# Kernel optimization log

Hardware: AMD Instinct MI355X
Metric: run time of the kernel (lower is better)

The kernel has to match this reference:

```python
import jax, jax.numpy as jnp
import numpy as np

B, L, D, H = 16, 1024, 768, 12
PHD = D // H  # per-head dim = 64


def setup_inputs() -> dict:
    key = jax.random.key(0)
    ks = jax.random.split(key, 6)
    s = 0.02  # small init scale (xavier-like magnitude)
    return {
        "embeddings": jax.random.normal(ks[0], (B, L, D), jnp.float32),
        "pre_w": jax.random.normal(ks[1], (D, D), jnp.float32) * s,
        "pre_b": jnp.zeros((D,), jnp.float32),
        "psfs": jax.random.normal(ks[2], (H, 2 * L - 1, PHD), jnp.float32) * s,
        "post_w": jax.random.normal(ks[3], (D, D), jnp.float32) * s,
        "post_b": jnp.zeros((D,), jnp.float32),
        "sparse_mat": jax.random.normal(ks[4], (L, L), jnp.float32) * s,
        "ln_g": jnp.ones((D,), jnp.float32),
        "ln_b": jnp.zeros((D,), jnp.float32),
    }


def _spectral_norm(W, n_iters=1, eps=1e-12):
    # torch spectral_norm: power iteration with detached u, v; sigma = u^T W v
    u = jnp.ones((W.shape[0],), W.dtype) / jnp.sqrt(jnp.asarray(W.shape[0], W.dtype))
    for _ in range(n_iters):
        v = W.T @ u
        v = v / (jnp.linalg.norm(v) + eps)
        u = W @ v
        u = u / (jnp.linalg.norm(u) + eps)
    u = jax.lax.stop_gradient(u)
    v = jax.lax.stop_gradient(v)
    sigma = u @ (W @ v)
    return W / sigma


def reference(embeddings, pre_w, pre_b, psfs, post_w, post_b, sparse_mat, ln_g, ln_b):
    # pre-projection
    x = embeddings @ pre_w.T + pre_b                       # (B, L, D)
    # zero-pad along seq to 2L-1 and split heads
    xp = jnp.pad(x, ((0, 0), (0, L - 1), (0, 0)))          # (B, 2L-1, D)
    xp = xp.reshape(B, 2 * L - 1, H, PHD).transpose(0, 2, 1, 3)  # (B, H, 2L-1, d)
    # causal PSF mask: keep first L taps, zero the rest (zeros still enter softmax, as in torch)
    causal = (jnp.arange(2 * L - 1) < L)[None, :, None]
    psf = jnp.where(causal, psfs, 0.0)                     # (H, 2L-1, d)
    psf = jax.nn.softmax(psf, axis=1)
    # 2D circular convolution via FFT over (seq, head_dim)
    conv = jnp.fft.ifftn(jnp.fft.fftn(psf, axes=(1, 2))[None] * jnp.fft.fftn(xp, axes=(2, 3)), axes=(2, 3))
    conv = jnp.real(conv)[:, :, :L, :]                     # (B, H, L, d)
    conv = jax.nn.gelu(conv, approximate=False).transpose(0, 2, 1, 3).reshape(B, L, D)
    conv_emb = conv @ post_w.T + post_b
    # sparse branch: spectrally-normalized, causal-masked dense mixing matrix
    sp = jnp.tril(_spectral_norm(sparse_mat))              # (L, L)
    sparse_emb = jnp.einsum('st,btd->bsd', sp, x)
    # dropout is identity (eval), keep_prob = 1.0; residual + LayerNorm(eps=1e-12)
    y = conv_emb + sparse_emb + embeddings
    mu = jnp.mean(y, axis=-1, keepdims=True)
    var = jnp.mean((y - mu) ** 2, axis=-1, keepdims=True)
    return (y - mu) * jax.lax.rsqrt(var + 1e-12) * ln_g + ln_b
```

## Files before the change

kernel.cpp:

```cpp
#include <hip/hip_runtime.h>
#include <math.h>

#define Bn 16
#define Ln 1024
#define Dn 768
#define Hn 12
#define PHDn 64
#define NK 33
#define NHK (Hn * NK)
#define TWOPI_64 0.09817477042468103f

typedef short s16x8 __attribute__((ext_vector_type(8)));
typedef float f32x4 __attribute__((ext_vector_type(4)));
typedef unsigned short u16x4 __attribute__((ext_vector_type(4)));

__device__ __forceinline__ unsigned short f2bf(float f) {
    unsigned int u = __float_as_uint(f);
    unsigned int r = (u + 0x7FFFu + ((u >> 16) & 1u)) >> 16;
    return (unsigned short)r;
}
__device__ __forceinline__ float bf2f(unsigned short s) {
    unsigned int u = ((unsigned int)s) << 16;
    return __uint_as_float(u);
}
__device__ __forceinline__ float2 cmul(float2 a, float2 b) {
    return make_float2(a.x * b.x - a.y * b.y, a.x * b.y + a.y * b.x);
}
__device__ __forceinline__ unsigned int packbf(float re, float im) {
    return (unsigned int)f2bf(re) | ((unsigned int)f2bf(im) << 16);
}
__device__ __forceinline__ float2 unpackbf(unsigned int v) {
    return make_float2(bf2f((unsigned short)(v & 0xffff)), bf2f((unsigned short)(v >> 16)));
}

#define SW(j) ((j) ^ (((j) >> 2) & 12) ^ (((j) >> 6) & 3))

static const size_t O_P    = 0;
static const size_t O_PSFH = 786432;
static const size_t O_PART = 1376256;
static const size_t O_QH   = 1597440;
static const size_t O_X    = 1598240;
static const size_t O_XH   = 14181152;
static const size_t O_YH   = 27157280;
static const size_t O_SPE  = 40146080;
static const size_t O_V    = 52728992;
static const size_t O_UR   = 52730016;
static const size_t O_SIG  = 52731040;

__global__ __launch_bounds__(256) void k_psf_softmax(const float* __restrict__ psfs,
                                                     float* __restrict__ p,
                                                     float* __restrict__ q) {
    int he = blockIdx.x;
    int h = he >> 6, e = he & 63;
    int tid = threadIdx.x;
    float ev[4];
    float s = 0.f;
#pragma unroll
    for (int i = 0; i < 4; ++i) {
        int t = tid + 256 * i;
        float v = psfs[((size_t)h * 2047 + t) * 64 + e];
        ev[i] = expf(v);
        s += ev[i];
    }
    __shared__ float red[256];
    red[tid] = s; __syncthreads();
    for (int st = 128; st > 0; st >>= 1) {
        if (tid < st) red[tid] += red[tid + st];
        __syncthreads();
    }
    float denom = red[0] + 1023.0f;
    float inv = 1.0f / denom;
#pragma unroll
    for (int i = 0; i < 4; ++i) {
        int t = tid + 256 * i;
        p[((size_t)h * 1024 + t) * 64 + e] = ev[i] * inv;
    }
    if (tid == 0) q[he] = inv;
}

__global__ __launch_bounds__(256) void k_psf_dft(const float* __restrict__ p,
                                                 float* __restrict__ psfh) {
    int blk = blockIdx.x;
    int h = blk >> 8, tb = blk & 255;
    int t0 = tb * 4;
    int tid = threadIdx.x;
    int w = tid >> 6, lane = tid & 63;
    __shared__ float pv[4][64], cc[64], ssn[64];
    if (tid < 64) {
        float ang = TWOPI_64 * tid;
        cc[tid] = cosf(ang); ssn[tid] = sinf(ang);
    }
    pv[w][lane] = p[((size_t)h * 1024 + t0 + w) * 64 + lane];
    __syncthreads();
    if (lane < NK) {
        float re = 0.f, im = 0.f;
#pragma unroll 8
        for (int e = 0; e < 64; ++e) {
            int j = (lane * e) & 63;
            float v = pv[w][e];
            re += v * cc[j];
            im -= v * ssn[j];
        }
        size_t o = (((size_t)h * NK + lane) * 1024 + t0 + w) * 2;
        psfh[o] = re; psfh[o + 1] = im;
    }
}

__global__ __launch_bounds__(64) void k_q_dft(const float* __restrict__ q,
                                              float* __restrict__ qh) {
    int h = blockIdx.x;
    int tid = threadIdx.x;
    __shared__ float qv[64], cc[64], ssn[64];
    qv[tid] = q[h * 64 + tid];
    float ang = TWOPI_64 * tid;
    cc[tid] = cosf(ang); ssn[tid] = sinf(ang);
    __syncthreads();
    if (tid < NK) {
        float re = 0.f, im = 0.f;
        for (int e = 0; e < 64; ++e) {
            int j = (tid * e) & 63;
            re += qv[e] * cc[j];
            im -= qv[e] * ssn[j];
        }
        qh[(h * NK + tid) * 2] = re;
        qh[(h * NK + tid) * 2 + 1] = im;
    }
}

__device__ __forceinline__ void build_twiddles(float2* tw, int tid) {
#pragma unroll
    for (int it = 0; it < 2; ++it) {
        int j = tid + it * 256;
        float a = (float)j * 3.0679615757712823e-3f;
        float sv, cv;
        __sincosf(a, &sv, &cv);
        tw[j] = make_float2(cv, -sv);
    }
}

__device__ __forceinline__ void fft_pair(const float2* __restrict__ X,
                                         float2* __restrict__ Y,
                                         const float2* __restrict__ tw,
                                         int tid, int m) {
#pragma unroll
    for (int it = 0; it < 2; ++it) {
        int i = tid + it * 256;
        int r = i & (m - 1);
        int am = i - r;
        float2 w1 = tw[am];
        float2 w1b = make_float2(w1.y, -w1.x);
        float2 w2 = cmul(w1, w1);
        float2 x0 = X[SW(i)], x1 = X[SW(i + 512)], x2 = X[SW(i + 1024)], x3 = X[SW(i + 1536)];
        float2 y0 = make_float2(x0.x + x2.x, x0.y + x2.y);
        float2 y1 = cmul(make_float2(x0.x - x2.x, x0.y - x2.y), w1);
        float2 y2 = make_float2(x1.x + x3.x, x1.y + x3.y);
        float2 y3 = cmul(make_float2(x1.x - x3.x, x1.y - x3.y), w1b);
        int o = 4 * am + r;
        Y[SW(o)] = make_float2(y0.x + y2.x, y0.y + y2.y);
        Y[SW(o + m)] = make_float2(y1.x + y3.x, y1.y + y3.y);
        Y[SW(o + 2 * m)] = cmul(make_float2(y0.x - y2.x, y0.y - y2.y), w2);
        Y[SW(o + 3 * m)] = cmul(make_float2(y1.x - y3.x, y1.y - y3.y), w2);
    }
}

__global__ __launch_bounds__(256) void k_tap_fft(const float* __restrict__ psfh,
                                                 const float* __restrict__ qh,
                                                 float* __restrict__ phf) {
    __shared__ float2 A[2048], B[2048], tw[512];
    int hk = blockIdx.x, tid = threadIdx.x;
    build_twiddles(tw, tid);
    float2 qv = make_float2(qh[hk * 2], qh[hk * 2 + 1]);
    const float2* Pg = (const float2*)(psfh + (size_t)hk * 2048);
    __syncthreads();
#pragma unroll
    for (int it = 0; it < 2; ++it) {
        int i = tid + it * 256;
        float2 x0 = Pg[i], x1 = Pg[i + 512];
        float2 x2 = (i == 0) ? make_float2(0.f, 0.f) : qv;
        float2 x3 = qv;
        float2 w1 = tw[i];
        float2 w1b = make_float2(w1.y, -w1.x);
        float2 w2 = cmul(w1, w1);
        float2 y0 = make_float2(x0.x + x2.x, x0.y + x2.y);
        float2 y1 = cmul(make_float2(x0.x - x2.x, x0.y - x2.y), w1);
        float2 y2 = make_float2(x1.x + x3.x, x1.y + x3.y);
        float2 y3 = cmul(make_float2(x1.x - x3.x, x1.y - x3.y), w1b);
        int o = 4 * i;
        A[SW(o)] = make_float2(y0.x + y2.x, y0.y + y2.y);
        A[SW(o + 1)] = make_float2(y1.x + y3.x, y1.y + y3.y);
        A[SW(o + 2)] = cmul(make_float2(y0.x - y2.x, y0.y - y2.y), w2);
        A[SW(o + 3)] = cmul(make_float2(y1.x - y3.x, y1.y - y3.y), w2);
    }
    __syncthreads();
    fft_pair(A, B, tw, tid, 4);   __syncthreads();
    fft_pair(B, A, tw, tid, 16);  __syncthreads();
    fft_pair(A, B, tw, tid, 64);  __syncthreads();
    fft_pair(B, A, tw, tid, 256); __syncthreads();
    float2* out = (float2*)(phf + (size_t)hk * 4096);
#pragma unroll
    for (int it = 0; it < 4; ++it) {
        int t = tid + it * 256;
        float2 lo = A[SW(t)], hi = A[SW(t + 1024)];
        out[t] = make_float2(lo.x + hi.x, lo.y + hi.y);
        out[t + 1024] = make_float2(lo.x - hi.x, lo.y - hi.y);
    }
}

__global__ __launch_bounds__(256) void k_conv_fft(const unsigned int* __restrict__ XHb,
                                                  const float* __restrict__ PHF,
                                                  unsigned int* __restrict__ YHb) {
    __shared__ float2 A[2048], B[2048], tw[512];
    int bhk = blockIdx.x, tid = threadIdx.x;
    int hk = bhk % NHK;
    build_twiddles(tw, tid);
    const unsigned int* Xg = XHb + (size_t)bhk * 1024;
    __syncthreads();
#pragma unroll
    for (int it = 0; it < 2; ++it) {
        int i = tid + it * 256;
        float2 x0 = unpackbf(Xg[i]);
        float2 x1 = unpackbf(Xg[i + 512]);
        float2 w1 = tw[i];
        float2 w1b = make_float2(w1.y, -w1.x);
        float2 w2 = cmul(w1, w1);
        float2 y1 = cmul(x0, w1);
        float2 y3 = cmul(x1, w1b);
        int o = 4 * i;
        A[SW(o)] = make_float2(x0.x + x1.x, x0.y + x1.y);
        A[SW(o + 1)] = make_float2(y1.x + y3.x, y1.y + y3.y);
        A[SW(o + 2)] = cmul(make_float2(x0.x - x1.x, x0.y - x1.y), w2);
        A[SW(o + 3)] = cmul(make_float2(y1.x - y3.x, y1.y - y3.y), w2);
    }
    __syncthreads();
    fft_pair(A, B, tw, tid, 4);   __syncthreads();
    fft_pair(B, A, tw, tid, 16);  __syncthreads();
    fft_pair(A, B, tw, tid, 64);  __syncthreads();
    fft_pair(B, A, tw, tid, 256); __syncthreads();
    const float2* P = (const float2*)(PHF + (size_t)hk * 4096);
    float2 q[8];
#pragma unroll
    for (int it = 0; it < 4; ++it) {
        int t = tid + it * 256;
        float2 lo = A[SW(t)], hi = A[SW(t + 1024)];
        float2 fl = make_float2(lo.x + hi.x, lo.y + hi.y);
        float2 fh = make_float2(lo.x - hi.x, lo.y - hi.y);
        float2 vl = cmul(fl, P[t]);
        float2 vh = cmul(fh, P[t + 1024]);
        q[it] = make_float2(vl.x, -vl.y);
        q[it + 4] = make_float2(vh.x, -vh.y);
    }
#pragma unroll
    for (int it = 0; it < 2; ++it) {
        int i = tid + it * 256;
        float2 x0 = q[it], x1 = q[it + 2], x2 = q[it + 4], x3 = q[it + 6];
        float2 w1 = tw[i];
        float2 w1b = make_float2(w1.y, -w1.x);
        float2 w2 = cmul(w1, w1);
        float2 y0 = make_float2(x0.x + x2.x, x0.y + x2.y);
        float2 y1 = cmul(make_float2(x0.x - x2.x, x0.y - x2.y), w1);
        float2 y2 = make_float2(x1.x + x3.x, x1.y + x3.y);
        float2 y3 = cmul(make_float2(x1.x - x3.x, x1.y - x3.y), w1b);
        int o = 4 * i;
        B[SW(o)] = make_float2(y0.x + y2.x, y0.y + y2.y);
        B[SW(o + 1)] = make_float2(y1.x + y3.x, y1.y + y3.y);
        B[SW(o + 2)] = cmul(make_float2(y0.x - y2.x, y0.y - y2.y), w2);
        B[SW(o + 3)] = cmul(make_float2(y1.x - y3.x, y1.y - y3.y), w2);
    }
    __syncthreads();
    fft_pair(B, A, tw, tid, 4);   __syncthreads();
    fft_pair(A, B, tw, tid, 16);  __syncthreads();
    fft_pair(B, A, tw, tid, 64);  __syncthreads();
    fft_pair(A, B, tw, tid, 256); __syncthreads();
    unsigned int* Yg = YHb + (size_t)bhk * 1024;
    const float inv_n = 1.0f / 2048.0f;
#pragma unroll
    for (int it = 0; it < 4; ++it) {
        int s = tid + it * 256;
        float2 lo = B[SW(s)], hi = B[SW(s + 1024)];
        Yg[s] = packbf((lo.x + hi.x) * inv_n, -(lo.y + hi.y) * inv_n);
    }
}

__global__ __launch_bounds__(64) void k_build_wf1(unsigned short* __restrict__ W) {
    int m = blockIdx.x;
    int d = threadIdx.x;
    float val = 0.f;
    if (m < 66) {
        int k = m >> 1, od = m & 1;
        int j = (k * d) & 63;
        float ang = TWOPI_64 * (float)j;
        val = od ? -sinf(ang) : cosf(ang);
    }
    W[m * 64 + d] = f2bf(val);
}

__global__ __launch_bounds__(64) void k_build_wi1(unsigned short* __restrict__ W) {
    int m = blockIdx.x;
    int c = threadIdx.x;
    float val = 0.f;
    if (m < 64) {
        int d = m;
        int k, od;
        float ck;
        if (c == 0)      { k = 0;  od = 0; ck = 1.f / 64.f; }
        else if (c == 1) { k = 32; od = 0; ck = 1.f / 64.f; }
        else             { k = c >> 1; od = c & 1; ck = 2.f / 64.f; }
        int j = (k * d) & 63;
        float ang = TWOPI_64 * (float)j;
        val = od ? -sinf(ang) * ck : cosf(ang) * ck;
    }
    W[m * 64 + c] = f2bf(val);
}

__device__ __forceinline__ void mfma_core64(const unsigned short* __restrict__ gA0,
                                            const unsigned short* __restrict__ gB0,
                                            int nkt,
                                            unsigned short* __restrict__ As,
                                            unsigned short* __restrict__ Bs,
                                            int tid, int lane, int wr, int wc,
                                            f32x4 acc[4][4]) {
    int r0 = tid >> 1, hs = (tid & 1) << 2;
    int wbase = r0 * 64;
    int swr = r0 & 7;
    int kg = lane >> 4, cl = lane & 15;
    int fra[8], frb[8];
#pragma unroll
    for (int kk = 0; kk < 2; ++kk)
#pragma unroll
        for (int i = 0; i < 4; ++i) {
            int ra = wr * 64 + i * 16 + cl;
            fra[kk * 4 + i] = ra * 64 + (((kk * 4 + kg) ^ (ra & 7)) << 3);
            int rb = wc * 64 + i * 16 + cl;
            frb[kk * 4 + i] = rb * 64 + (((kk * 4 + kg) ^ (rb & 7)) << 3);
        }
    s16x8 a[4], b[4];
#pragma unroll
    for (int l = 0; l < 4; ++l) {
        a[l] = *(const s16x8*)(gA0 + l * 8);
        b[l] = *(const s16x8*)(gB0 + l * 8);
    }
    for (int kt = 0; kt < nkt; ++kt) {
        __syncthreads();
#pragma unroll
        for (int l = 0; l < 4; ++l) {
            *(s16x8*)&As[wbase + (((hs + l) ^ swr) << 3)] = a[l];
            *(s16x8*)&Bs[wbase + (((hs + l) ^ swr) << 3)] = b[l];
        }
        __syncthreads();
        if (kt + 1 < nkt) {
            size_t ko = (size_t)(kt + 1) * 64;
#pragma unroll
            for (int l = 0; l < 4; ++l) {
                a[l] = *(const s16x8*)(gA0 + ko + l * 8);
                b[l] = *(const s16x8*)(gB0 + ko + l * 8);
            }
        }
#pragma unroll
        for (int kk = 0; kk < 2; ++kk) {
            s16x8 af[4], bfr[4];
#pragma unroll
            for (int i = 0; i < 4; ++i) af[i] = *(const s16x8*)&As[fra[kk * 4 + i]];
#pragma unroll
            for (int i = 0; i < 4; ++i) bfr[i] = *(const s16x8*)&Bs[frb[kk * 4 + i]];
#pragma unroll
            for (int mi = 0; mi < 4; ++mi)
#pragma unroll
                for (int ni = 0; ni < 4; ++ni)
                    acc[mi][ni] = __builtin_amdgcn_mfma_f32_16x16x32_bf16(af[mi], bfr[ni], acc[mi][ni], 0, 0, 0);
        }
    }
}

__global__ __launch_bounds__(512) void k_mfma_proj(const unsigned short* __restrict__ A,
                                                   const unsigned short* __restrict__ W,
                                                   const float* __restrict__ bias,
                                                   unsigned short* __restrict__ C) {
    const int K = Dn, N = Dn;
    int n0 = blockIdx.x * 256, m0 = blockIdx.y * 128;
    int tid = threadIdx.x;
    int lane = tid & 63, wave = tid >> 6;
    int wr = wave >> 2, wc = wave & 3;
    __shared__ __align__(16) unsigned short As[8192], Bs[16384];
    f32x4 acc[4][4] = {};
    int ra0 = tid >> 2, sa0 = (tid & 3) * 2;
    int rb0 = tid >> 1, sb0 = (tid & 1) * 4;
    const unsigned short* gA = A + (size_t)(m0 + ra0) * K + sa0 * 8;
    const unsigned short* gB = W + (size_t)(n0 + rb0) * K + sb0 * 8;
    int kg = lane >> 4, cl = lane & 15;
    int fra[8], frb[8];
#pragma unroll
    for (int kk = 0; kk < 2; ++kk)
#pragma unroll
        for (int i = 0; i < 4; ++i) {
            int ra = wr * 64 + i * 16 + cl;
            fra[kk * 4 + i] = ra * 64 + (((kk * 4 + kg) ^ (ra & 7)) << 3);
            int rb = wc * 64 + i * 16 + cl;
            frb[kk * 4 + i] = rb * 64 + (((kk * 4 + kg) ^ (rb & 7)) << 3);
        }
    s16x8 a[2], b[4];
#pragma unroll
    for (int l = 0; l < 2; ++l) a[l] = *(const s16x8*)(gA + l * 8);
#pragma unroll
    for (int l = 0; l < 4; ++l) b[l] = *(const s16x8*)(gB + l * 8);
    const int nkt = K >> 6;
    for (int kt = 0; kt < nkt; ++kt) {
        __syncthreads();
#pragma unroll
        for (int l = 0; l < 2; ++l)
            *(s16x8*)&As[ra0 * 64 + (((sa0 + l) ^ (ra0 & 7)) << 3)] = a[l];
#pragma unroll
        for (int l = 0; l < 4; ++l)
            *(s16x8*)&Bs[rb0 * 64 + (((sb0 + l) ^ (rb0 & 7)) << 3)] = b[l];
        __syncthreads();
        if (kt + 1 < nkt) {
            size_t ko = (size_t)(kt + 1) * 64;
#pragma unroll
            for (int l = 0; l < 2; ++l) a[l] = *(const s16x8*)(gA + ko + l * 8);
#pragma unroll
            for (int l = 0; l < 4; ++l) b[l] = *(const s16x8*)(gB + ko + l * 8);
        }
#pragma unroll
        for (int kk = 0; kk < 2; ++kk) {
            s16x8 af[4], bfr[4];
#pragma unroll
            for (int i = 0; i < 4; ++i) af[i] = *(const s16x8*)&As[fra[kk * 4 + i]];
#pragma unroll
            for (int i = 0; i < 4; ++i) bfr[i] = *(const s16x8*)&Bs[frb[kk * 4 + i]];
#pragma unroll
            for (int mi = 0; mi < 4; ++mi)
#pragma unroll
                for (int ni = 0; ni < 4; ++ni)
                    acc[mi][ni] = __builtin_amdgcn_mfma_f32_16x16x32_bf16(af[mi], bfr[ni], acc[mi][ni], 0, 0, 0);
        }
    }
#pragma unroll
    for (int ni = 0; ni < 4; ++ni) {
        int gn = n0 + wc * 64 + ni * 16 + cl;
        float bv = bias[gn];
#pragma unroll
        for (int mi = 0; mi < 4; ++mi) {
            int gm = m0 + wr * 64 + mi * 16 + kg * 4;
            f32x4 v = acc[mi][ni];
#pragma unroll
            for (int ri = 0; ri < 4; ++ri)
                C[(size_t)(gm + ri) * N + gn] = f2bf(v[ri] + bv);
        }
    }
}

__global__ __launch_bounds__(256) void k_mfma_dft_h(const unsigned short* __restrict__ Wf1,
                                                    const unsigned short* __restrict__ Xb,
                                                    unsigned int* __restrict__ XHb) {
    int n0 = blockIdx.x * 128;
    int h = blockIdx.y;
    int tid = threadIdx.x;
    int lane = tid & 63, wave = tid >> 6;
    int wr = wave >> 1, wc = wave & 1;
    __shared__ __align__(16) unsigned short As[8192], Bs[8192];
    f32x4 acc[4][4] = {};
    int r0 = tid >> 1, hs = (tid & 1) << 2;
    const unsigned short* gA0 = Wf1 + r0 * 64 + hs * 8;
    const unsigned short* gB0 = Xb + (size_t)(n0 + r0) * Dn + h * 64 + hs * 8;
    mfma_core64(gA0, gB0, 1, As, Bs, tid, lane, wr, wc, acc);
    int kg = lane >> 4, cl = lane & 15;
#pragma unroll
    for (int ni = 0; ni < 4; ++ni) {
        int gn = n0 + wc * 64 + ni * 16 + cl;
        int b = gn >> 10, u = gn & 1023;
#pragma unroll
        for (int mi = 0; mi < 4; ++mi) {
            int gmb = wr * 64 + mi * 16 + kg * 4;
            f32x4 v = acc[mi][ni];
#pragma unroll
            for (int rp = 0; rp < 2; ++rp) {
                int m = gmb + rp * 2;
                if (m < 66) {
                    size_t plane = (size_t)(b * Hn + h) * NK + (m >> 1);
                    XHb[plane * 1024 + u] = packbf(v[rp * 2], v[rp * 2 + 1]);
                }
            }
        }
    }
}

__global__ __launch_bounds__(256) void k_transpose_yh(const unsigned int* __restrict__ YHb,
                                                      unsigned short* __restrict__ YT) {
    int ut = blockIdx.x & 7;
    int h = (blockIdx.x >> 3) % 12;
    int b = blockIdx.x / 96;
    int u0 = ut * 128;
    __shared__ unsigned short T[128 * 66];
    int tid = threadIdx.x;
    int planeBase = (b * Hn + h) * NK;
#pragma unroll
    for (int i = 0; i < 17; ++i) {
        int idx = tid + i * 256;
        if (idx < 4224) {
            int k = idx >> 7, uo = idx & 127;
            unsigned int v = YHb[(size_t)(planeBase + k) * 1024 + u0 + uo];
            T[uo * 66 + 2 * k] = (unsigned short)(v & 0xffff);
            T[uo * 66 + 2 * k + 1] = (unsigned short)(v >> 16);
        }
    }
    __syncthreads();
    unsigned int* out = (unsigned int*)YT;
#pragma unroll
    for (int i = 0; i < 16; ++i) {
        int idx = tid + i * 256;
        int uo = idx >> 5, w = idx & 31;
        unsigned int lo, hi;
        if (w == 0) {
            lo = T[uo * 66 + 0];
            hi = T[uo * 66 + 64];
        } else {
            lo = T[uo * 66 + 2 * w];
            hi = T[uo * 66 + 2 * w + 1];
        }
        size_t r = (size_t)b * 1024 + u0 + uo;
        out[r * 384 + h * 32 + w] = lo | (hi << 16);
    }
}

__global__ __launch_bounds__(256) void k_mfma_idft_h(const unsigned short* __restrict__ YT,
                                                     const unsigned short* __restrict__ Wi1,
                                                     unsigned short* __restrict__ G) {
    int m0 = blockIdx.x * 128;
    int h = blockIdx.y;
    int tid = threadIdx.x;
    int lane = tid & 63, wave = tid >> 6;
    int wr = wave >> 1, wc = wave & 1;
    __shared__ __align__(16) unsigned short As[8192], Bs[8192];
    f32x4 acc[4][4] = {};
    int r0 = tid >> 1, hs = (tid & 1) << 2;
    const unsigned short* gA0 = YT + (size_t)(m0 + r0) * Dn + h * 64 + hs * 8;
    const unsigned short* gB0 = Wi1 + r0 * 64 + hs * 8;
    mfma_core64(gA0, gB0, 1, As, Bs, tid, lane, wr, wc, acc);
    int kg = lane >> 4, cl = lane & 15;
#pragma unroll
    for (int ni = 0; ni < 4; ++ni) {
        int gn = wc * 64 + ni * 16 + cl;
        if (gn < 64) {
#pragma unroll
            for (int mi = 0; mi < 4; ++mi) {
                int gm = m0 + wr * 64 + mi * 16 + kg * 4;
                f32x4 v = acc[mi][ni];
#pragma unroll
                for (int ri = 0; ri < 4; ++ri) {
                    float c = v[ri];
                    float g = c * 0.5f * (1.0f + erff(c * 0.70710678118f));
                    G[(size_t)(gm + ri) * Dn + h * 64 + gn] = f2bf(g);
                }
            }
        }
    }
}

__global__ __launch_bounds__(256) void k_mfma_sparse(const unsigned short* __restrict__ SP,
                                                     const unsigned short* __restrict__ XT,
                                                     const float* __restrict__ sigbuf,
                                                     unsigned short* __restrict__ C) {
    int bx = blockIdx.x;
    int mt = bx & 7, nt = (bx >> 3) % 6, b = bx / 48;
    int m0 = mt * 128, n0 = nt * 128;
    const unsigned short* Xb = XT + (size_t)b * Dn * Ln;
    unsigned short* Cb = C + (size_t)b * Ln * Dn;
    int tid = threadIdx.x;
    int lane = tid & 63, wave = tid >> 6;
    int wr = wave >> 1, wc = wave & 1;
    __shared__ __align__(16) unsigned short As[8192], Bs[8192];
    f32x4 acc[4][4] = {};
    int r0 = tid >> 1, hs = (tid & 1) << 2;
    const unsigned short* gA0 = SP + (size_t)(m0 + r0) * Ln + hs * 8;
    const unsigned short* gB0 = Xb + (size_t)(n0 + r0) * Ln + hs * 8;
    mfma_core64(gA0, gB0, 2 * mt + 2, As, Bs, tid, lane, wr, wc, acc);
    float invs = sigbuf[0];
    int kg = lane >> 4, cl = lane & 15;
#pragma unroll
    for (int ni = 0; ni < 4; ++ni) {
        int gn = n0 + wc * 64 + ni * 16 + cl;
#pragma unroll
        for (int mi = 0; mi < 4; ++mi) {
            int gm = m0 + wr * 64 + mi * 16 + kg * 4;
            f32x4 v = acc[mi][ni];
#pragma unroll
            for (int ri = 0; ri < 4; ++ri)
                Cb[(size_t)(gm + ri) * Dn + gn] = f2bf(v[ri] * invs);
        }
    }
}

__global__ __launch_bounds__(256) void k_cvt_bf16(const float* __restrict__ in,
                                                  unsigned short* __restrict__ out, int n4) {
    int i = blockIdx.x * 256 + threadIdx.x;
    if (i < n4) {
        float4 v = ((const float4*)in)[i];
        u16x4 o;
        o[0] = f2bf(v.x); o[1] = f2bf(v.y); o[2] = f2bf(v.z); o[3] = f2bf(v.w);
        *(u16x4*)&out[(size_t)i * 4] = o;
    }
}

__global__ __launch_bounds__(256) void k_cvt_sp(const float* __restrict__ SP,
                                                unsigned short* __restrict__ O) {
    int s = blockIdx.x;
    int t0 = threadIdx.x * 4;
    float4 v = *(const float4*)&SP[(size_t)s * 1024 + t0];
    u16x4 o;
    o[0] = (t0 + 0 <= s) ? f2bf(v.x) : 0;
    o[1] = (t0 + 1 <= s) ? f2bf(v.y) : 0;
    o[2] = (t0 + 2 <= s) ? f2bf(v.z) : 0;
    o[3] = (t0 + 3 <= s) ? f2bf(v.w) : 0;
    *(u16x4*)&O[(size_t)s * 1024 + t0] = o;
}

__global__ __launch_bounds__(256) void k_transpose_x(const unsigned short* __restrict__ X,
                                                     unsigned short* __restrict__ XT) {
    int d0 = blockIdx.x * 64, t0 = blockIdx.y * 64, b = blockIdx.z;
    const unsigned short* Xb = X + (size_t)b * Ln * Dn;
    unsigned short* Tb = XT + (size_t)b * Dn * Ln;
    __shared__ unsigned short tile[64 * 65];
    int tx = threadIdx.x & 63, ty = threadIdx.x >> 6;
#pragma unroll
    for (int i = 0; i < 16; ++i) {
        int t = ty + i * 4;
        tile[t * 65 + tx] = Xb[(size_t)(t0 + t) * Dn + d0 + tx];
    }
    __syncthreads();
#pragma unroll
    for (int i = 0; i < 16; ++i) {
        int d = ty + i * 4;
        Tb[(size_t)(d0 + d) * Ln + t0 + tx] = tile[tx * 65 + d];
    }
}

__global__ __launch_bounds__(256) void k_sn_colsum(const float* __restrict__ Wm,
                                                   float* __restrict__ partial) {
    int b = blockIdx.x;
    int tid = threadIdx.x;
    int c0 = tid * 4;
    float4 s = make_float4(0.f, 0.f, 0.f, 0.f);
#pragma unroll
    for (int i = 0; i < 16; ++i) {
        float4 v = *(const float4*)&Wm[(size_t)(b * 16 + i) * 1024 + c0];
        s.x += v.x; s.y += v.y; s.z += v.z; s.w += v.w;
    }
    *(float4*)&partial[(size_t)b * 1024 + c0] = s;
}

__global__ __launch_bounds__(1024) void k_sn_v2(const float* __restrict__ partial,
                                                float* __restrict__ v) {
    int j = threadIdx.x;
    float s = 0.f;
#pragma unroll 8
    for (int i = 0; i < 64; ++i) s += partial[(size_t)i * 1024 + j];
    s *= 0.03125f;
    __shared__ float red[1024];
    red[j] = s * s; __syncthreads();
    for (int st = 512; st > 0; st >>= 1) {
        if (j < st) red[j] += red[j + st];
        __syncthreads();
    }
    float nrm = sqrtf(red[0]);
    v[j] = s / (nrm + 1e-12f);
}

__global__ __launch_bounds__(64) void k_sn_u(const float* __restrict__ Wm,
                                             const float* __restrict__ v,
                                             float* __restrict__ ur) {
    int i = blockIdx.x;
    int lane = threadIdx.x;
    float s = 0.f;
    for (int j = lane; j < 1024; j += 64) s += Wm[(size_t)i * 1024 + j] * v[j];
#pragma unroll
    for (int off = 32; off > 0; off >>= 1) s += __shfl_down(s, off);
    if (lane == 0) ur[i] = s;
}

__global__ __launch_bounds__(1024) void k_sn_sigma(const float* __restrict__ ur,
                                                   float* __restrict__ sig) {
    int i = threadIdx.x;
    __shared__ float red[1024];
    float u = ur[i];
    red[i] = u * u; __syncthreads();
    for (int st = 512; st > 0; st >>= 1) {
        if (i < st) red[i] += red[i + st];
        __syncthreads();
    }
    if (i == 0) {
        float ss = red[0];
        float sigma = ss / (sqrtf(ss) + 1e-12f);
        sig[0] = 1.0f / sigma;
    }
}

__global__ __launch_bounds__(256) void k_final_ln(const unsigned short* __restrict__ CE,
                                                  const unsigned short* __restrict__ SE,
                                                  const float* __restrict__ EMB,
                                                  const float* __restrict__ g,
                                                  const float* __restrict__ be,
                                                  float* __restrict__ out) {
    int r = blockIdx.x;
    int tid = threadIdx.x;
    float y[3];
    float s = 0.f;
#pragma unroll
    for (int i = 0; i < 3; ++i) {
        int o = tid + i * 256;
        size_t idx = (size_t)r * 768 + o;
        y[i] = bf2f(CE[idx]) + bf2f(SE[idx]) + EMB[idx];
        s += y[i];
    }
    __shared__ float red[256];
    red[tid] = s; __syncthreads();
    for (int st = 128; st > 0; st >>= 1) {
        if (tid < st) red[tid] += red[tid + st];
        __syncthreads();
    }
    float mu = red[0] * (1.f / 768.f);
    __syncthreads();
    float vs = 0.f;
#pragma unroll
    for (int i = 0; i < 3; ++i) { float d = y[i] - mu; vs += d * d; }
    red[tid] = vs; __syncthreads();
    for (int st = 128; st > 0; st >>= 1) {
        if (tid < st) red[tid] += red[tid + st];
        __syncthreads();
    }
    float var = red[0] * (1.f / 768.f);
    float rstd = rsqrtf(var + 1e-12f);
#pragma unroll
    for (int i = 0; i < 3; ++i) {
        int o = tid + i * 256;
        size_t idx = (size_t)r * 768 + o;
        out[idx] = (y[i] - mu) * rstd * g[o] + be[o];
    }
}

extern "C" void kernel_launch(void* const* d_in, const int* in_sizes, int n_in,
                              void* d_out, int out_size, void* d_ws, size_t ws_size,
                              hipStream_t stream) {
    const float* emb     = (const float*)d_in[0];
    const float* pre_w   = (const float*)d_in[1];
    const float* pre_b   = (const float*)d_in[2];
    const float* psfs    = (const float*)d_in[3];
    const float* post_w  = (const float*)d_in[4];
    const float* post_b  = (const float*)d_in[5];
    const float* spmat   = (const float*)d_in[6];
    const float* ln_g    = (const float*)d_in[7];
    const float* ln_b    = (const float*)d_in[8];
    float* out = (float*)d_out;
    float* ws = (float*)d_ws;

    float* p      = ws + O_P;
    float* psfh   = ws + O_PSFH;
    float* part   = ws + O_PART;
    float* qh     = ws + O_QH;
    float* q      = ws + O_SIG + 8;
    unsigned int* XHb = (unsigned int*)(ws + O_XH);
    unsigned int* YHb = (unsigned int*)(ws + O_YH);
    float* phf    = ws + O_SPE;
    float* v      = ws + O_V;
    float* urw    = ws + O_UR;
    float* sig    = ws + O_SIG;

    unsigned short* x_bf      = (unsigned short*)(ws + O_X);
    unsigned short* Wf1       = (unsigned short*)(ws + O_X + 6291456);
    unsigned short* Wi1       = (unsigned short*)(ws + O_X + 6295552);
    unsigned short* YT        = (unsigned short*)(ws + O_XH);
    unsigned short* xT_bf     = (unsigned short*)(ws + O_XH);
    unsigned short* emb_bf    = (unsigned short*)(ws + O_YH);
    unsigned short* CE_bf     = (unsigned short*)(ws + O_YH);
    unsigned short* spe_bf    = (unsigned short*)(ws + O_SPE);
    unsigned short* G_bf      = (unsigned short*)(ws + O_SPE + 3145728);
    unsigned short* SP_bf     = (unsigned short*)(ws + O_P);
    unsigned short* pre_w_bf  = (unsigned short*)(ws + O_PSFH);
    unsigned short* post_w_bf = (unsigned short*)(ws + O_PSFH + 294912);

    k_psf_softmax<<<Hn * 64, 256, 0, stream>>>(psfs, p, q);
    k_psf_dft<<<Hn * 256, 256, 0, stream>>>(p, psfh);
    k_q_dft<<<Hn, 64, 0, stream>>>(q, qh);
    k_tap_fft<<<NHK, 256, 0, stream>>>(psfh, qh, phf);

    k_sn_colsum<<<64, 256, 0, stream>>>(spmat, part);
    k_sn_v2<<<1, 1024, 0, stream>>>(part, v);
    k_sn_u<<<1024, 64, 0, stream>>>(spmat, v, urw);
    k_sn_sigma<<<1, 1024, 0, stream>>>(urw, sig);

    k_cvt_sp<<<1024, 256, 0, stream>>>(spmat, SP_bf);
    k_cvt_bf16<<<576, 256, 0, stream>>>(pre_w, pre_w_bf, 147456);
    k_cvt_bf16<<<576, 256, 0, stream>>>(post_w, post_w_bf, 147456);
    k_cvt_bf16<<<12288, 256, 0, stream>>>(emb, emb_bf, 3145728);
    k_build_wf1<<<128, 64, 0, stream>>>(Wf1);
    k_build_wi1<<<128, 64, 0, stream>>>(Wi1);

    k_mfma_proj<<<dim3(3, 128), 512, 0, stream>>>(emb_bf, pre_w_bf, pre_b, x_bf);

    k_mfma_dft_h<<<dim3(128, Hn), 256, 0, stream>>>(Wf1, x_bf, XHb);

    k_conv_fft<<<Bn * NHK, 256, 0, stream>>>(XHb, phf, YHb);

    k_transpose_yh<<<Bn * Hn * 8, 256, 0, stream>>>(YHb, YT);

    k_mfma_idft_h<<<dim3(128, Hn), 256, 0, stream>>>(YT, Wi1, G_bf);

    k_transpose_x<<<dim3(12, 16, Bn), 256, 0, stream>>>(x_bf, xT_bf);

    k_mfma_proj<<<dim3(3, 128), 512, 0, stream>>>(G_bf, post_w_bf, post_b, CE_bf);

    k_mfma_sparse<<<768, 256, 0, stream>>>(SP_bf, xT_bf, sig, spe_bf);

    k_final_ln<<<Bn * Ln, 256, 0, stream>>>(CE_bf, spe_bf, emb, ln_g, ln_b, out);
}
```

Measured before the change: 315.4 us.

## Restructure conv FFT into radix-8 register passes with padded single shared buffer

Rewrites the per-(b,h,k) 2048-point FFT convolution kernel to use radix-8 register-resident passes (three stages plus a final radix-4) instead of radix-4 ping-pong passes through two shared arrays. This cuts the number of shared-memory round trips and barriers per FFT. The A/B ping-pong becomes one shared buffer with skew padding in place of the XOR swizzle, which lowers LDS footprint and may allow more resident blocks. The inverse pass computes only the first 1024 outputs it needs. Register pressure per thread rises, which may hurt occupancy.

```diff
diff --git a/kernel.cpp b/kernel.cpp
--- a/kernel.cpp
+++ b/kernel.cpp
@@ -26,6 +26,8 @@
 __device__ __forceinline__ float2 cmul(float2 a, float2 b) {
     return make_float2(a.x * b.x - a.y * b.y, a.x * b.y + a.y * b.x);
 }
+__device__ __forceinline__ float2 cadd(float2 a, float2 b) { return make_float2(a.x + b.x, a.y + b.y); }
+__device__ __forceinline__ float2 csub(float2 a, float2 b) { return make_float2(a.x - b.x, a.y - b.y); }
 __device__ __forceinline__ unsigned int packbf(float re, float im) {
     return (unsigned int)f2bf(re) | ((unsigned int)f2bf(im) << 16);
 }
@@ -34,6 +36,7 @@
 }
 
 #define SW(j) ((j) ^ (((j) >> 2) & 12) ^ (((j) >> 6) & 3))
+#define PD(j) ((j) + ((j) >> 4))
 
 static const size_t O_P    = 0;
 static const size_t O_PSFH = 786432;
@@ -151,15 +154,15 @@
         float2 w1b = make_float2(w1.y, -w1.x);
         float2 w2 = cmul(w1, w1);
         float2 x0 = X[SW(i)], x1 = X[SW(i + 512)], x2 = X[SW(i + 1024)], x3 = X[SW(i + 1536)];
-        float2 y0 = make_float2(x0.x + x2.x, x0.y + x2.y);
-        float2 y1 = cmul(make_float2(x0.x - x2.x, x0.y - x2.y), w1);
-        float2 y2 = make_float2(x1.x + x3.x, x1.y + x3.y);
-        float2 y3 = cmul(make_float2(x1.x - x3.x, x1.y - x3.y), w1b);
+        float2 y0 = cadd(x0, x2);
+        float2 y1 = cmul(csub(x0, x2), w1);
+        float2 y2 = cadd(x1, x3);
+        float2 y3 = cmul(csub(x1, x3), w1b);
         int o = 4 * am + r;
-        Y[SW(o)] = make_float2(y0.x + y2.x, y0.y + y2.y);
-        Y[SW(o + m)] = make_float2(y1.x + y3.x, y1.y + y3.y);
-        Y[SW(o + 2 * m)] = cmul(make_float2(y0.x - y2.x, y0.y - y2.y), w2);
-        Y[SW(o + 3 * m)] = cmul(make_float2(y1.x - y3.x, y1.y - y3.y), w2);
+        Y[SW(o)] = cadd(y0, y2);
+        Y[SW(o + m)] = cadd(y1, y3);
+        Y[SW(o + 2 * m)] = cmul(csub(y0, y2), w2);
+        Y[SW(o + 3 * m)] = cmul(csub(y1, y3), w2);
     }
 }
 
@@ -181,15 +184,15 @@
         float2 w1 = tw[i];
         float2 w1b = make_float2(w1.y, -w1.x);
         float2 w2 = cmul(w1, w1);
-        float2 y0 = make_float2(x0.x + x2.x, x0.y + x2.y);
-        float2 y1 = cmul(make_float2(x0.x - x2.x, x0.y - x2.y), w1);
-        float2 y2 = make_float2(x1.x + x3.x, x1.y + x3.y);
-        float2 y3 = cmul(make_float2(x1.x - x3.x, x1.y - x3.y), w1b);
+        float2 y0 = cadd(x0, x2);
+        float2 y1 = cmul(csub(x0, x2), w1);
+        float2 y2 = cadd(x1, x3);
+        float2 y3 = cmul(csub(x1, x3), w1b);
         int o = 4 * i;
-        A[SW(o)] = make_float2(y0.x + y2.x, y0.y + y2.y);
-        A[SW(o + 1)] = make_float2(y1.x + y3.x, y1.y + y3.y);
-        A[SW(o + 2)] = cmul(make_float2(y0.x - y2.x, y0.y - y2.y), w2);
-        A[SW(o + 3)] = cmul(make_float2(y1.x - y3.x, y1.y - y3.y), w2);
+        A[SW(o)] = cadd(y0, y2);
+        A[SW(o + 1)] = cadd(y1, y3);
+        A[SW(o + 2)] = cmul(csub(y0, y2), w2);
+        A[SW(o + 3)] = cmul(csub(y1, y3), w2);
     }
     __syncthreads();
     fft_pair(A, B, tw, tid, 4);   __syncthreads();
@@ -201,83 +204,146 @@
     for (int it = 0; it < 4; ++it) {
         int t = tid + it * 256;
         float2 lo = A[SW(t)], hi = A[SW(t + 1024)];
-        out[t] = make_float2(lo.x + hi.x, lo.y + hi.y);
-        out[t + 1024] = make_float2(lo.x - hi.x, lo.y - hi.y);
-    }
+        out[t] = cadd(lo, hi);
+        out[t + 1024] = csub(lo, hi);
+    }
+}
+
+__device__ __forceinline__ void triple_tail(float2 z0, float2 z1, float2 z2, float2 z3,
+                                            float2 zz0, float2 zz1, float2 zz2, float2 zz3,
+                                            float2 w2, float2 w4, float2* o) {
+    float2 w2b = make_float2(w2.y, -w2.x);
+    float2 a0 = cadd(z0, z2),   a2 = cmul(csub(z0, z2), w2);
+    float2 b0 = cadd(z1, z3),   b2 = cmul(csub(z1, z3), w2b);
+    float2 a1 = cadd(zz0, zz2), a3 = cmul(csub(zz0, zz2), w2);
+    float2 b1 = cadd(zz1, zz3), b3 = cmul(csub(zz1, zz3), w2b);
+    o[0] = cadd(a0, b0); o[4] = cmul(csub(a0, b0), w4);
+    o[1] = cadd(a1, b1); o[5] = cmul(csub(a1, b1), w4);
+    o[2] = cadd(a2, b2); o[6] = cmul(csub(a2, b2), w4);
+    o[3] = cadd(a3, b3); o[7] = cmul(csub(a3, b3), w4);
+}
+
+__device__ __forceinline__ void fft_triple(const float2* x, float2 w10, float2 w11, float2* o) {
+    float2 w10b = make_float2(w10.y, -w10.x), w11b = make_float2(w11.y, -w11.x);
+    float2 w2 = cmul(w10, w10), w4 = cmul(w2, w2);
+    float2 z0 = cadd(x[0], x[4]), z1 = cadd(x[1], x[5]);
+    float2 z2 = cadd(x[2], x[6]), z3 = cadd(x[3], x[7]);
+    float2 zz0 = cmul(csub(x[0], x[4]), w10);
+    float2 zz1 = cmul(csub(x[1], x[5]), w11);
+    float2 zz2 = cmul(csub(x[2], x[6]), w10b);
+    float2 zz3 = cmul(csub(x[3], x[7]), w11b);
+    triple_tail(z0, z1, z2, z3, zz0, zz1, zz2, zz3, w2, w4, o);
 }
 
 __global__ __launch_bounds__(256) void k_conv_fft(const unsigned int* __restrict__ XHb,
                                                   const float* __restrict__ PHF,
                                                   unsigned int* __restrict__ YHb) {
-    __shared__ float2 A[2048], B[2048], tw[512];
+    __shared__ float2 S[2176], tw[512];
     int bhk = blockIdx.x, tid = threadIdx.x;
     int hk = bhk % NHK;
     build_twiddles(tw, tid);
     const unsigned int* Xg = XHb + (size_t)bhk * 1024;
-    __syncthreads();
+    float2 x[8], o[8];
+#pragma unroll
+    for (int k = 0; k < 4; ++k) x[k] = unpackbf(Xg[tid + 256 * k]);
+    __syncthreads();
+    {
+        float2 w10 = tw[tid], w11 = tw[tid + 256];
+        float2 w10b = make_float2(w10.y, -w10.x), w11b = make_float2(w11.y, -w11.x);
+        float2 w2 = cmul(w10, w10), w4 = cmul(w2, w2);
+        float2 zz0 = cmul(x[0], w10), zz1 = cmul(x[1], w11);
+        float2 zz2 = cmul(x[2], w10b), zz3 = cmul(x[3], w11b);
+        triple_tail(x[0], x[1], x[2], x[3], zz0, zz1, zz2, zz3, w2, w4, o);
+    }
+#pragma unroll
+    for (int k = 0; k < 8; ++k) S[PD(8 * tid + k)] = o[k];
+    __syncthreads();
+    {
+        int r = tid & 7, am = tid - r;
+#pragma unroll
+        for (int k = 0; k < 8; ++k) x[k] = S[PD(tid + 256 * k)];
+        __syncthreads();
+        fft_triple(x, tw[am], tw[am + 256], o);
+        int base = 8 * am + r;
+#pragma unroll
+        for (int k = 0; k < 8; ++k) S[PD(base + 8 * k)] = o[k];
+    }
+    __syncthreads();
+    {
+        int r = tid & 63, am = tid - r;
+#pragma unroll
+        for (int k = 0; k < 8; ++k) x[k] = S[PD(tid + 256 * k)];
+        __syncthreads();
+        fft_triple(x, tw[am], tw[am + 256], o);
+        int base = 8 * am + r;
+#pragma unroll
+        for (int k = 0; k < 8; ++k) S[PD(base + 64 * k)] = o[k];
+    }
+    __syncthreads();
+    const float2* P = (const float2*)(PHF + (size_t)hk * 4096);
+    float2 v[8];
 #pragma unroll
     for (int it = 0; it < 2; ++it) {
-        int i = tid + it * 256;
-        float2 x0 = unpackbf(Xg[i]);
-        float2 x1 = unpackbf(Xg[i + 512]);
-        float2 w1 = tw[i];
-        float2 w1b = make_float2(w1.y, -w1.x);
-        float2 w2 = cmul(w1, w1);
-        float2 y1 = cmul(x0, w1);
-        float2 y3 = cmul(x1, w1b);
-        int o = 4 * i;
-        A[SW(o)] = make_float2(x0.x + x1.x, x0.y + x1.y);
-        A[SW(o + 1)] = make_float2(y1.x + y3.x, y1.y + y3.y);
-        A[SW(o + 2)] = cmul(make_float2(x0.x - x1.x, x0.y - x1.y), w2);
-        A[SW(o + 3)] = cmul(make_float2(y1.x - y3.x, y1.y - y3.y), w2);
-    }
-    __syncthreads();
-    fft_pair(A, B, tw, tid, 4);   __syncthreads();
-    fft_pair(B, A, tw, tid, 16);  __syncthreads();
-    fft_pair(A, B, tw, tid, 64);  __syncthreads();
-    fft_pair(B, A, tw, tid, 256); __syncthreads();
-    const float2* P = (const float2*)(PHF + (size_t)hk * 4096);
-    float2 q[8];
-#pragma unroll
-    for (int it = 0; it < 4; ++it) {
-        int t = tid + it * 256;
-        float2 lo = A[SW(t)], hi = A[SW(t + 1024)];
-        float2 fl = make_float2(lo.x + hi.x, lo.y + hi.y);
-        float2 fh = make_float2(lo.x - hi.x, lo.y - hi.y);
-        float2 vl = cmul(fl, P[t]);
-        float2 vh = cmul(fh, P[t + 1024]);
-        q[it] = make_float2(vl.x, -vl.y);
-        q[it + 4] = make_float2(vh.x, -vh.y);
-    }
-#pragma unroll
-    for (int it = 0; it < 2; ++it) {
-        int i = tid + it * 256;
-        float2 x0 = q[it], x1 = q[it + 2], x2 = q[it + 4], x3 = q[it + 6];
-        float2 w1 = tw[i];
-        float2 w1b = make_float2(w1.y, -w1.x);
-        float2 w2 = cmul(w1, w1);
-        float2 y0 = make_float2(x0.x + x2.x, x0.y + x2.y);
-        float2 y1 = cmul(make_float2(x0.x - x2.x, x0.y - x2.y), w1);
-        float2 y2 = make_float2(x1.x + x3.x, x1.y + x3.y);
-        float2 y3 = cmul(make_float2(x1.x - x3.x, x1.y - x3.y), w1b);
-        int o = 4 * i;
-        B[SW(o)] = make_float2(y0.x + y2.x, y0.y + y2.y);
-        B[SW(o + 1)] = make_float2(y1.x + y3.x, y1.y + y3.y);
-        B[SW(o + 2)] = cmul(make_float2(y0.x - y2.x, y0.y - y2.y), w2);
-        B[SW(o + 3)] = cmul(make_float2(y1.x - y3.x, y1.y - y3.y), w2);
-    }
-    __syncthreads();
-    fft_pair(B, A, tw, tid, 4);   __syncthreads();
-    fft_pair(A, B, tw, tid, 16);  __syncthreads();
-    fft_pair(B, A, tw, tid, 64);  __syncthreads();
-    fft_pair(A, B, tw, tid, 256); __syncthreads();
+        int i2 = tid + 256 * it;
+        float2 g0 = S[PD(i2)], g1 = S[PD(i2 + 512)], g2 = S[PD(i2 + 1024)], g3 = S[PD(i2 + 1536)];
+        float2 y0 = cadd(g0, g2), y1 = csub(g0, g2);
+        float2 y2 = cadd(g1, g3);
+        float2 d13 = csub(g1, g3);
+        float2 y3 = make_float2(d13.y, -d13.x);
+        float2 F0 = cadd(y0, y2);
+        float2 F1 = cadd(y1, y3);
+        float2 F2 = csub(y0, y2);
+        float2 F3 = csub(y1, y3);
+        float2 V0 = cmul(F0, P[i2]);
+        float2 V1 = cmul(F1, P[i2 + 512]);
+        float2 V2 = cmul(F2, P[i2 + 1024]);
+        float2 V3 = cmul(F3, P[i2 + 1536]);
+        v[it]     = make_float2(V0.x, -V0.y);
+        v[it + 2] = make_float2(V1.x, -V1.y);
+        v[it + 4] = make_float2(V2.x, -V2.y);
+        v[it + 6] = make_float2(V3.x, -V3.y);
+    }
+    __syncthreads();
+    fft_triple(v, tw[tid], tw[tid + 256], o);
+#pragma unroll
+    for (int k = 0; k < 8; ++k) S[PD(8 * tid + k)] = o[k];
+    __syncthreads();
+    {
+        int r = tid & 7, am = tid - r;
+#pragma unroll
+        for (int k = 0; k < 8; ++k) x[k] = S[PD(tid + 256 * k)];
+        __syncthreads();
+        fft_triple(x, tw[am], tw[am + 256], o);
+        int base = 8 * am + r;
+#pragma unroll
+        for (int k = 0; k < 8; ++k) S[PD(base + 8 * k)] = o[k];
+    }
+    __syncthreads();
+    {
+        int r = tid & 63, am = tid - r;
+#pragma unroll
+        for (int k = 0; k < 8; ++k) x[k] = S[PD(tid + 256 * k)];
+        __syncthreads();
+        fft_triple(x, tw[am], tw[am + 256], o);
+        int base = 8 * am + r;
+#pragma unroll
+        for (int k = 0; k < 8; ++k) S[PD(base + 64 * k)] = o[k];
+    }
+    __syncthreads();
     unsigned int* Yg = YHb + (size_t)bhk * 1024;
     const float inv_n = 1.0f / 2048.0f;
 #pragma unroll
-    for (int it = 0; it < 4; ++it) {
-        int s = tid + it * 256;
-        float2 lo = B[SW(s)], hi = B[SW(s + 1024)];
-        Yg[s] = packbf((lo.x + hi.x) * inv_n, -(lo.y + hi.y) * inv_n);
+    for (int it = 0; it < 2; ++it) {
+        int i2 = tid + 256 * it;
+        float2 g0 = S[PD(i2)], g1 = S[PD(i2 + 512)], g2 = S[PD(i2 + 1024)], g3 = S[PD(i2 + 1536)];
+        float2 s02 = cadd(g0, g2), d02 = csub(g0, g2);
+        float2 s13 = cadd(g1, g3);
+        float2 d13 = csub(g1, g3);
+        float2 mj13 = make_float2(d13.y, -d13.x);
+        float2 o0 = cadd(s02, s13);
+        float2 o1 = cadd(d02, mj13);
+        Yg[i2] = packbf(o0.x * inv_n, -o0.y * inv_n);
+        Yg[i2 + 512] = packbf(o1.x * inv_n, -o1.y * inv_n);
     }
 }
 
```

After: 310.9 us. About the same (-1.4%).
